# Kernel tuning notes

Hardware: AMD Instinct MI355X
Metric: run time of the kernel (lower is better)

The kernel has to match this reference:

```python
import jax, jax.numpy as jnp
from jax import lax
import numpy as np

FEAT_STRIDE = 16
RATIOS = np.array([0.5, 1.0, 2.0])
SCALES = np.array([8.0, 16.0, 32.0])
PRE_NMS = 6000
POST_NMS = 300
NMS_THRESH = 0.7
MIN_SIZE = 16.0
A = 9  # num anchors per location


def _whctrs(a):
    w = a[2] - a[0] + 1.0
    h = a[3] - a[1] + 1.0
    return w, h, a[0] + 0.5 * (w - 1.0), a[1] + 0.5 * (h - 1.0)


def _mkanchors(ws, hs, cx, cy):
    return np.stack([cx - 0.5 * (ws - 1.0), cy - 0.5 * (hs - 1.0),
                     cx + 0.5 * (ws - 1.0), cy + 0.5 * (hs - 1.0)], axis=1)


def generate_anchors(base_size=16):
    base = np.array([1.0, 1.0, base_size, base_size]) - 1.0
    w, h, cx, cy = _whctrs(base)
    size = w * h
    ws = np.round(np.sqrt(size / RATIOS))
    hs = np.round(ws * RATIOS)
    ratio_anchors = _mkanchors(ws, hs, cx, cy)
    out = []
    for ra in ratio_anchors:
        w, h, cx, cy = _whctrs(ra)
        out.append(_mkanchors(w * SCALES, h * SCALES, cx, cy))
    return np.concatenate(out, axis=0).astype(np.float32)  # [9,4]


def setup_inputs() -> dict:
    key = jax.random.key(0)
    k1, k2 = jax.random.split(key)
    scores = jax.random.normal(k1, (1, 2 * A, 50, 80), dtype=jnp.float32)
    bbox_deltas = jax.random.normal(k2, (1, 4 * A, 50, 80), dtype=jnp.float32) * 0.5
    im_info = jnp.array([[800.0, 1280.0, 1.5]], dtype=jnp.float32)  # (h, w, scale)
    return {"scores": scores, "bbox_deltas": bbox_deltas, "im_info": im_info}


def reference(scores, bbox_deltas, im_info):
    base_anchors = jnp.asarray(generate_anchors())  # [A,4]
    H, W = scores.shape[-2], scores.shape[-1]

    # fg scores, flattened in (h, w, a) order to match anchor ordering
    sc = scores[:, A:, :, :].transpose(0, 2, 3, 1).reshape(-1)  # [K*A]

    # anchors for every feature-map location
    sx = (jnp.arange(W) * FEAT_STRIDE).astype(jnp.float32)
    sy = (jnp.arange(H) * FEAT_STRIDE).astype(jnp.float32)
    gy, gx = jnp.meshgrid(sy, sx, indexing="ij")
    shifts = jnp.stack([gx, gy, gx, gy], axis=-1).reshape(-1, 1, 4)  # [K,1,4]
    anchors = (base_anchors[None, :, :] + shifts).reshape(-1, 4)    # [K*A,4]

    # decode deltas (dw/dh clamped to [-10,10])
    d = bbox_deltas.transpose(0, 2, 3, 1).reshape(-1, 4)
    d = jnp.concatenate([d[:, :2], jnp.clip(d[:, 2:], -10.0, 10.0)], axis=1)
    aw = anchors[:, 2] - anchors[:, 0] + 1.0
    ah = anchors[:, 3] - anchors[:, 1] + 1.0
    acx = anchors[:, 0] + 0.5 * aw
    acy = anchors[:, 1] + 0.5 * ah
    pcx = d[:, 0] * aw + acx
    pcy = d[:, 1] * ah + acy
    pw = jnp.exp(d[:, 2]) * aw
    ph = jnp.exp(d[:, 3]) * ah
    boxes = jnp.stack([pcx - 0.5 * pw, pcy - 0.5 * ph,
                       pcx + 0.5 * pw, pcy + 0.5 * ph], axis=1)

    # clip to image
    im_h, im_w, im_s = im_info[0, 0], im_info[0, 1], im_info[0, 2]
    boxes = jnp.stack([
        jnp.clip(boxes[:, 0], 0.0, im_w - 1.0),
        jnp.clip(boxes[:, 1], 0.0, im_h - 1.0),
        jnp.clip(boxes[:, 2], 0.0, im_w - 1.0),
        jnp.clip(boxes[:, 3], 0.0, im_h - 1.0),
    ], axis=1)

    # min-size filter (masking instead of compaction, for static shapes)
    ws = boxes[:, 2] - boxes[:, 0] + 1.0
    hs = boxes[:, 3] - boxes[:, 1] + 1.0
    min_sz = MIN_SIZE * im_s
    valid = (ws >= min_sz) & (hs >= min_sz)
    sc = jnp.where(valid, sc, -jnp.inf)

    # pre-NMS top-k by score
    top_sc, top_idx = lax.top_k(sc, PRE_NMS)
    props = boxes[top_idx]  # [P,4], sorted by descending score
    alive0 = jnp.isfinite(top_sc)

    # pairwise IoU (the +1 pixel convention matching the rest of the pipeline)
    x1, y1, x2, y2 = props[:, 0], props[:, 1], props[:, 2], props[:, 3]
    areas = (x2 - x1 + 1.0) * (y2 - y1 + 1.0)
    iw = jnp.clip(jnp.minimum(x2[:, None], x2[None, :]) - jnp.maximum(x1[:, None], x1[None, :]) + 1.0, 0.0)
    ih = jnp.clip(jnp.minimum(y2[:, None], y2[None, :]) - jnp.maximum(y1[:, None], y1[None, :]) + 1.0, 0.0)
    inter = iw * ih
    iou = inter / (areas[:, None] + areas[None, :] - inter)  # [P,P] ~144MB

    idx = jnp.arange(PRE_NMS)

    def body(i, keep):
        sup = keep[i] & (iou[i] > NMS_THRESH) & (idx > i)
        return keep & ~sup

    keep = lax.fori_loop(0, PRE_NMS, body, alive0)

    # gather first POST_NMS kept proposals into fixed-size output [POST_NMS,5]
    rank = jnp.cumsum(keep) - 1
    dest = jnp.where(keep & (rank < POST_NMS), rank, POST_NMS)
    out = jnp.zeros((POST_NMS + 1, 5), dtype=scores.dtype)
    out = out.at[dest, 1:].set(props)
    return out[:POST_NMS]
```

## Files before the change

### kernel.cpp

```cpp
#include <hip/hip_runtime.h>
#include <stdint.h>

#define A_NUM 9
#define H_FM 50
#define W_FM 80
#define HW (H_FM * W_FM)
#define N_ANCH (A_NUM * HW)
#define PRE_NMS_N 6000
#define POST_NMS_N 300
#define NMS_TH 0.7f
#define MASK_W 94
#define NPAIR 47
#define MASK_STRIDE 96
#define NBIN 4096
#define BIN_CAP 4096
#define NBD 141
#define MASK_TILES (24 * 94)

typedef unsigned long long ull;

__constant__ float c_aw[9] = {184.f,368.f,736.f,128.f,256.f,512.f, 88.f,176.f,352.f};
__constant__ float c_ah[9] = { 96.f,192.f,384.f,128.f,256.f,512.f,176.f,352.f,704.f};

__device__ int    g_hist[NBIN];
__device__ ull    g_dead[MASK_STRIDE];
__device__ ull    g_rowany[MASK_STRIDE];
__device__ float4 g_boxes[N_ANCH];
__device__ float4 g_props[PRE_NMS_N];
__device__ ull    g_mask[(size_t)PRE_NMS_N * MASK_STRIDE];
__device__ ull    g_colsup[MASK_W * 64];
__device__ ull    g_csup[NPAIR * 64];

__device__ __forceinline__ float iou_gt(float4 bi, float ai, float4 bj, float aj) {
    float iw = fminf(bi.z, bj.z) - fmaxf(bi.x, bj.x) + 1.f;
    float ih = fminf(bi.w, bj.w) - fmaxf(bi.y, bj.y) + 1.f;
    iw = fmaxf(iw, 0.f);
    ih = fmaxf(ih, 0.f);
    float inter = iw * ih;
    return inter / (ai + aj - inter);
}

__global__ __launch_bounds__(256) void k_decode(const float* __restrict__ scores,
                                                const float* __restrict__ deltas,
                                                const float* __restrict__ iminfo,
                                                ull* __restrict__ bins) {
    int t = blockIdx.x * 256 + threadIdx.x;
    if (t >= N_ANCH) return;
    int a    = t / HW;
    int cell = t - a * HW;
    int x    = cell % W_FM;
    int y    = cell / W_FM;

    float sc = scores[(A_NUM + a) * HW + cell];

    int dbase = (a * 4) * HW + cell;
    float d0 = deltas[dbase];
    float d1 = deltas[dbase + HW];
    float d2 = deltas[dbase + 2 * HW];
    float d3 = deltas[dbase + 3 * HW];
    d2 = fminf(fmaxf(d2, -10.f), 10.f);
    d3 = fminf(fmaxf(d3, -10.f), 10.f);

    float aw = c_aw[a], ah = c_ah[a];
    float acx = (float)(x * 16 + 8);
    float acy = (float)(y * 16 + 8);

    float pcx = d0 * aw + acx;
    float pcy = d1 * ah + acy;
    float pw  = expf(d2) * aw;
    float ph  = expf(d3) * ah;

    float x1 = pcx - 0.5f * pw;
    float y1 = pcy - 0.5f * ph;
    float x2 = pcx + 0.5f * pw;
    float y2 = pcy + 0.5f * ph;

    float imh = iminfo[0], imw = iminfo[1], ims = iminfo[2];
    x1 = fminf(fmaxf(x1, 0.f), imw - 1.f);
    y1 = fminf(fmaxf(y1, 0.f), imh - 1.f);
    x2 = fminf(fmaxf(x2, 0.f), imw - 1.f);
    y2 = fminf(fmaxf(y2, 0.f), imh - 1.f);

    float wsz = x2 - x1 + 1.f;
    float hsz = y2 - y1 + 1.f;
    float minsz = 16.f * ims;
    bool valid = (wsz >= minsz) && (hsz >= minsz);

    g_boxes[t] = make_float4(x1, y1, x2, y2);

    unsigned int u   = __float_as_uint(sc);
    unsigned int asc = (u & 0x80000000u) ? ~u : (u | 0x80000000u);
    unsigned int dk  = ~asc;
    if (!valid) dk = 0xFF800000u;

    unsigned int ikey = (unsigned int)(cell * A_NUM + a);
    ull key = ((ull)dk << 32) | ikey;

    int bin  = (int)(dk >> 20);
    int slot = atomicAdd(&g_hist[bin], 1);
    if (slot < BIN_CAP) bins[(size_t)bin * BIN_CAP + slot] = key;
}

__global__ __launch_bounds__(256) void k_binsort(const ull* __restrict__ bins) {
    __shared__ ull sb[4096];
    __shared__ int red[256];
    int b = blockIdx.x;
    int cntf = g_hist[b];
    if (cntf == 0) return;
    int tid = threadIdx.x;

    int part = 0;
    for (int j = tid; j < b; j += 256) part += g_hist[j];
    red[tid] = part;
    __syncthreads();
    for (int off = 128; off > 0; off >>= 1) {
        if (tid < off) red[tid] += red[tid + off];
        __syncthreads();
    }
    int s0 = red[0];
    if (s0 >= PRE_NMS_N) return;

    int cnt = (cntf < BIN_CAP) ? cntf : BIN_CAP;
    const ull* seg = bins + (size_t)b * BIN_CAP;

    int P = 2; while (P < cnt) P <<= 1;
    for (int i = tid; i < P; i += 256) sb[i] = (i < cnt) ? seg[i] : ~0ULL;
    __syncthreads();
    for (int k2 = 2; k2 <= P; k2 <<= 1) {
        for (int j = k2 >> 1; j >= 1; j >>= 1) {
            for (int p = tid; p < (P >> 1); p += 256) {
                int i  = ((p & ~(j - 1)) << 1) | (p & (j - 1));
                int pr = i | j;
                bool up = ((i & k2) == 0);
                ull a = sb[i], c = sb[pr];
                if ((a > c) == up) { sb[i] = c; sb[pr] = a; }
            }
            __syncthreads();
        }
    }
    for (int i = tid; i < cnt; i += 256) {
        int r = s0 + i;
        if (r < PRE_NMS_N) {
            ull key = sb[i];
            unsigned int dk = (unsigned int)(key >> 32);
            if (dk < 0xFF800000u) {
                unsigned int ik = (unsigned int)key;
                int tt = (int)(ik % A_NUM) * HW + (int)(ik / A_NUM);
                g_props[r] = g_boxes[tt];
            } else {
                g_props[r] = make_float4(0.f, 0.f, 0.f, 0.f);
                atomicOr(&g_dead[r >> 6], 1ULL << (r & 63));
            }
        }
    }
}

__global__ __launch_bounds__(256) void k_maskcol() {
    __shared__ float4 sj[256];
    int vb = blockIdx.x;
    int tid = threadIdx.x;

    if (vb < 16) g_hist[vb * 256 + tid] = 0;

    if (vb < MASK_TILES) {
        int bx = vb % 24;
        int by = vb / 24;

        int li = tid & 63;
        int wl = tid >> 6;
        int i  = by * 64 + li;
        int w  = bx * 4 + wl;

        if (bx * 256 + 255 <= by * 64) {
            if (i < PRE_NMS_N && w < MASK_W)
                g_mask[(size_t)i * MASK_STRIDE + w] = 0ULL;
            return;
        }

        int jbase = bx * 256;
        int jj = jbase + tid;
        sj[tid] = (jj < PRE_NMS_N) ? g_props[jj] : make_float4(0.f, 0.f, 0.f, 0.f);
        __syncthreads();

        if (i >= PRE_NMS_N || w >= MASK_W) return;

        float4 bi = g_props[i];
        float ai = (bi.z - bi.x + 1.f) * (bi.w - bi.y + 1.f);
        ull bits = 0;
        int jstart = w * 64;
        int lbase = jstart - jbase;
        int bstart = i + 1 - jstart; if (bstart < 0) bstart = 0;
        int bend = PRE_NMS_N - jstart; if (bend > 64) bend = 64;
        for (int b = bstart; b < bend; ++b) {
            float4 bj = sj[lbase + b];
            float aj = (bj.z - bj.x + 1.f) * (bj.w - bj.y + 1.f);
            if (iou_gt(bi, ai, bj, aj) > NMS_TH) bits |= (1ULL << b);
        }
        g_mask[(size_t)i * MASK_STRIDE + w] = bits;
        int wi = i >> 6;
        bool instep = (w == wi) || (((wi & 1) == 0) && (w == wi + 1));
        if (bits && !instep) atomicOr(&g_rowany[wi], 1ULL << (i & 63));
    } else {
        int w = vb - MASK_TILES;
        int gj = w * 64 + tid;
        if (tid < 64)
            sj[tid] = (gj < PRE_NMS_N) ? g_props[gj] : make_float4(0.f, 0.f, 0.f, 0.f);
        if ((w & 1) && tid >= 64 && tid < 128) {
            int gj2 = (w - 1) * 64 + (tid - 64);
            sj[tid] = (gj2 < PRE_NMS_N) ? g_props[gj2] : make_float4(0.f, 0.f, 0.f, 0.f);
        }
        __syncthreads();
        if (tid < 64) {
            float4 bj = sj[tid];
            float aj = (bj.z - bj.x + 1.f) * (bj.w - bj.y + 1.f);
            ull bits = 0;
            for (int b = 0; b < tid; ++b) {
                float4 bi = sj[b];
                float ai = (bi.z - bi.x + 1.f) * (bi.w - bi.y + 1.f);
                if (iou_gt(bi, ai, bj, aj) > NMS_TH) bits |= (1ULL << b);
            }
            g_colsup[gj] = bits;
            if (w & 1) {
                ull cb = 0;
                for (int b = 0; b < 64; ++b) {
                    float4 bi = sj[64 + b];
                    float ai = (bi.z - bi.x + 1.f) * (bi.w - bi.y + 1.f);
                    if (iou_gt(bi, ai, bj, aj) > NMS_TH) cb |= (1ULL << b);
                }
                g_csup[(w >> 1) * 64 + tid] = cb;
            }
        }
    }
}

#define BATCH 8
__global__ __launch_bounds__(256, 1) void k_scan(float* __restrict__ out) {
    __shared__ ull scol[MASK_W * 64];
    __shared__ ull scsup[NPAIR * 64];
    __shared__ ull srow[MASK_W];
    __shared__ int s_kept[POST_NMS_N];
    __shared__ int s_kc;
    int tid = threadIdx.x;

    for (int i = tid; i < MASK_W * 64; i += 256) scol[i] = g_colsup[i];
    for (int i = tid; i < NPAIR * 64; i += 256)  scsup[i] = g_csup[i];
    for (int i = tid; i < MASK_W; i += 256)      srow[i] = g_rowany[i];
    __syncthreads();

    if (tid < 64) {
        int lane = tid;
        ull rm0 = g_dead[lane];
        ull rm1 = (lane < MASK_W - 64) ? g_dead[64 + lane] : ~0ULL;
        if (lane == 29) rm1 |= 0xFFFF000000000000ULL;
        int kc = 0;
        int ps = -2;
        ull pA = 0, pB = 0, pC = 0;

        for (;;) {
            ull avail0 = __ballot(~rm0 != 0ULL);
            ull avail1 = __ballot(~rm1 != 0ULL);
            int w;
            if (avail0)      w = __ffsll(avail0) - 1;
            else if (avail1) w = 63 + __ffsll(avail1);
            else break;

            int s  = w >> 1;
            int w0 = s << 1;
            int w1 = w0 | 1;

            ull diagA, diagB, csup;
            if (s == ps + 1) { diagA = pA; diagB = pB; csup = pC; }
            else {
                diagA = scol[(w0 << 6) + lane];
                diagB = scol[(w1 << 6) + lane];
                csup  = scsup[(s << 6) + lane];
            }
            if (s + 1 < NPAIR) {
                pA = scol[((w0 + 2) << 6) + lane];
                pB = scol[((w1 + 2) << 6) + lane];
                pC = scsup[((s + 1) << 6) + lane];
            }
            ps = s;

            ull raw0 = srow[w0], raw1 = srow[w1];

            ull rmw0 = (w0 < 64) ? rm0 : rm1;
            int ri0  = (w0 < 64) ? w0 : w0 - 64;
            ull curw0 = ((ull)__builtin_amdgcn_readlane((unsigned)(rmw0 >> 32), ri0) << 32)
                        | __builtin_amdgcn_readlane((unsigned)rmw0, ri0);
            ull rmw1 = (w1 < 64) ? rm0 : rm1;
            int ri1  = (w1 < 64) ? w1 : w1 - 64;
            ull curw1 = ((ull)__builtin_amdgcn_readlane((unsigned)(rmw1 >> 32), ri1) << 32)
                        | __builtin_amdgcn_readlane((unsigned)rmw1, ri1);

            ull U = ~curw0, K0 = 0;
            while (U) {
                ull UK = U | K0;
                bool deadp = (diagA & K0) != 0ULL;
                bool freep = (diagA & UK) == 0ULL;
                ull nd = __ballot(deadp) & U;
                U &= ~nd;
                ull nk = __ballot(freep) & U;
                U &= ~nk;
                K0 |= nk;
                if (!nk && !nd) break;
            }

            ull U1 = ~curw1;
            U1 &= ~__ballot((csup & K0) != 0ULL);
            ull K1 = 0;
            while (U1) {
                ull UK = U1 | K1;
                bool deadp = (diagB & K1) != 0ULL;
                bool freep = (diagB & UK) == 0ULL;
                ull nd = __ballot(deadp) & U1;
                U1 &= ~nd;
                ull nk = __ballot(freep) & U1;
                U1 &= ~nk;
                K1 |= nk;
                if (!nk && !nd) break;
            }

            int cnt0 = __popcll(K0);
            int take0 = min(cnt0, POST_NMS_N - kc);
            if (K0 & (1ULL << lane)) {
                int pos = kc + __popcll(K0 & ((1ULL << lane) - 1ULL));
                if (pos < POST_NMS_N) s_kept[pos] = (w0 << 6) + lane;
            }
            kc += take0;
            if (kc >= POST_NMS_N) break;

            int cnt1 = __popcll(K1);
            int take1 = min(cnt1, POST_NMS_N - kc);
            if (K1 & (1ULL << lane)) {
                int pos = kc + __popcll(K1 & ((1ULL << lane) - 1ULL));
                if (pos < POST_NMS_N) s_kept[pos] = (w1 << 6) + lane;
            }
            kc += take1;
            if (kc >= POST_NMS_N) break;

            if (w0 < 64) { if (lane == w0)      rm0 = ~0ULL; }
            else         { if (lane == w0 - 64) rm1 = ~0ULL; }
            if (w1 < 64) { if (lane == w1)      rm0 = ~0ULL; }
            else         { if (lane == w1 - 64) rm1 = ~0ULL; }

            ull needA = K0 & raw0;
            ull needB = K1 & raw1;
            while (needA | needB) {
                int id[BATCH];
                int n = 0;
#pragma unroll
                for (int t2 = 0; t2 < BATCH; ++t2) {
                    id[t2] = 0;
                    if (needA) {
                        int b = __ffsll(needA) - 1; needA &= needA - 1;
                        id[t2] = (w0 << 6) + b; n = t2 + 1;
                    } else if (needB) {
                        int b = __ffsll(needB) - 1; needB &= needB - 1;
                        id[t2] = (w1 << 6) + b; n = t2 + 1;
                    }
                }
                ull v0[BATCH], v1[BATCH];
#pragma unroll
                for (int t2 = 0; t2 < BATCH; ++t2) {
                    const ull* __restrict__ row =
                        g_mask + (size_t)id[t2] * MASK_STRIDE;
                    v0[t2] = row[lane];
                    v1[t2] = (lane < MASK_W - 64) ? row[64 + lane] : 0ULL;
                }
                ull a0 = 0, a1 = 0;
#pragma unroll
                for (int t2 = 0; t2 < BATCH; ++t2) {
                    ull m = (t2 < n) ? ~0ULL : 0ULL;
                    a0 |= v0[t2] & m;
                    a1 |= v1[t2] & m;
                }
                rm0 |= a0;
                rm1 |= a1;
            }
        }
        if (lane == 0) s_kc = (kc < POST_NMS_N) ? kc : POST_NMS_N;
    }
    __syncthreads();

    for (int i = tid; i < MASK_STRIDE; i += 256) {
        g_dead[i] = 0ULL;
        g_rowany[i] = 0ULL;
    }

    int kcf = s_kc;
    for (int r = tid; r < POST_NMS_N; r += 256) {
        float4 p = make_float4(0.f, 0.f, 0.f, 0.f);
        if (r < kcf) p = g_props[s_kept[r]];
        out[r * 5 + 0] = 0.f;
        out[r * 5 + 1] = p.x;
        out[r * 5 + 2] = p.y;
        out[r * 5 + 3] = p.z;
        out[r * 5 + 4] = p.w;
    }
}

extern "C" void kernel_launch(void* const* d_in, const int* in_sizes, int n_in,
                              void* d_out, int out_size, void* d_ws, size_t ws_size,
                              hipStream_t stream) {
    const float* scores = (const float*)d_in[0];
    const float* deltas = (const float*)d_in[1];
    const float* iminfo = (const float*)d_in[2];
    float* out = (float*)d_out;
    ull* bins = (ull*)d_ws;

    k_decode<<<NBD, 256, 0, stream>>>(scores, deltas, iminfo, bins);
    k_binsort<<<NBIN, 256, 0, stream>>>(bins);
    k_maskcol<<<MASK_TILES + MASK_W, 256, 0, stream>>>();
    k_scan<<<1, 256, 0, stream>>>(out);
}
```

Before: 122.3 us.

## Remap mask tile threads, precompute areas in LDS, aggregate row flags

Rearranges the IoU mask tile kernel so each group of four adjacent threads handles one row across four 64-bit mask words. This makes the global mask stores contiguous. Candidate box areas are computed once into a padded shared array instead of being recomputed inside every inner loop. Lower-triangle tiles now exit without writing zeros, which relies on those mask entries staying zero from static initialisation. Per-row any-suppression bits are gathered with a shared-memory atomic and flushed once per block, instead of one global atomic per thread.

Measured after the change: 119.5 us. -2.3%, faster.

```diff
diff --git a/kernel.cpp b/kernel.cpp
--- a/kernel.cpp
+++ b/kernel.cpp
@@ -31,7 +31,7 @@
 __device__ ull    g_colsup[MASK_W * 64];
 __device__ ull    g_csup[NPAIR * 64];
 
-__device__ __forceinline__ float iou_gt(float4 bi, float ai, float4 bj, float aj) {
+__device__ __forceinline__ float iou_of(float4 bi, float ai, float4 bj, float aj) {
     float iw = fminf(bi.z, bj.z) - fmaxf(bi.x, bj.x) + 1.f;
     float ih = fminf(bi.w, bj.w) - fmaxf(bi.y, bj.y) + 1.f;
     iw = fmaxf(iw, 0.f);
@@ -156,7 +156,9 @@
 }
 
 __global__ __launch_bounds__(256) void k_maskcol() {
-    __shared__ float4 sj[256];
+    __shared__ float4 sj[4 * 65];
+    __shared__ float  sa[4 * 65];
+    __shared__ ull    s_row;
     int vb = blockIdx.x;
     int tid = threadIdx.x;
 
@@ -166,40 +168,43 @@
         int bx = vb % 24;
         int by = vb / 24;
 
-        int li = tid & 63;
-        int wl = tid >> 6;
+        if (bx * 256 + 255 <= by * 64) return;
+
+        if (tid == 0) s_row = 0ULL;
+
+        int li = tid >> 2;
+        int wl = tid & 3;
         int i  = by * 64 + li;
         int w  = bx * 4 + wl;
 
-        if (bx * 256 + 255 <= by * 64) {
-            if (i < PRE_NMS_N && w < MASK_W)
-                g_mask[(size_t)i * MASK_STRIDE + w] = 0ULL;
-            return;
-        }
-
+        int q = tid >> 6, r = tid & 63;
         int jbase = bx * 256;
-        int jj = jbase + tid;
-        sj[tid] = (jj < PRE_NMS_N) ? g_props[jj] : make_float4(0.f, 0.f, 0.f, 0.f);
+        int jj = jbase + q * 64 + r;
+        float4 bjs = (jj < PRE_NMS_N) ? g_props[jj] : make_float4(0.f, 0.f, 0.f, 0.f);
+        sj[q * 65 + r] = bjs;
+        sa[q * 65 + r] = (bjs.z - bjs.x + 1.f) * (bjs.w - bjs.y + 1.f);
         __syncthreads();
 
-        if (i >= PRE_NMS_N || w >= MASK_W) return;
-
-        float4 bi = g_props[i];
-        float ai = (bi.z - bi.x + 1.f) * (bi.w - bi.y + 1.f);
+        bool act = (i < PRE_NMS_N) && (w < MASK_W);
         ull bits = 0;
-        int jstart = w * 64;
-        int lbase = jstart - jbase;
-        int bstart = i + 1 - jstart; if (bstart < 0) bstart = 0;
-        int bend = PRE_NMS_N - jstart; if (bend > 64) bend = 64;
-        for (int b = bstart; b < bend; ++b) {
-            float4 bj = sj[lbase + b];
-            float aj = (bj.z - bj.x + 1.f) * (bj.w - bj.y + 1.f);
-            if (iou_gt(bi, ai, bj, aj) > NMS_TH) bits |= (1ULL << b);
-        }
-        g_mask[(size_t)i * MASK_STRIDE + w] = bits;
+        if (act) {
+            float4 bi = g_props[i];
+            float ai = (bi.z - bi.x + 1.f) * (bi.w - bi.y + 1.f);
+            int jstart = w * 64;
+            int bstart = i + 1 - jstart; if (bstart < 0) bstart = 0;
+            int bend = PRE_NMS_N - jstart; if (bend > 64) bend = 64;
+            const float4* sw = &sj[wl * 65];
+            const float*  swa = &sa[wl * 65];
+            for (int b = bstart; b < bend; ++b) {
+                if (iou_of(bi, ai, sw[b], swa[b]) > NMS_TH) bits |= (1ULL << b);
+            }
+            g_mask[(size_t)i * MASK_STRIDE + w] = bits;
+        }
         int wi = i >> 6;
         bool instep = (w == wi) || (((wi & 1) == 0) && (w == wi + 1));
-        if (bits && !instep) atomicOr(&g_rowany[wi], 1ULL << (i & 63));
+        if (act && bits && !instep) atomicOr(&s_row, 1ULL << (i & 63));
+        __syncthreads();
+        if (tid == 0 && s_row) atomicOr(&g_rowany[by], s_row);
     } else {
         int w = vb - MASK_TILES;
         int gj = w * 64 + tid;
@@ -217,7 +222,7 @@
             for (int b = 0; b < tid; ++b) {
                 float4 bi = sj[b];
                 float ai = (bi.z - bi.x + 1.f) * (bi.w - bi.y + 1.f);
-                if (iou_gt(bi, ai, bj, aj) > NMS_TH) bits |= (1ULL << b);
+                if (iou_of(bi, ai, bj, aj) > NMS_TH) bits |= (1ULL << b);
             }
             g_colsup[gj] = bits;
             if (w & 1) {
@@ -225,7 +230,7 @@
                 for (int b = 0; b < 64; ++b) {
                     float4 bi = sj[64 + b];
                     float ai = (bi.z - bi.x + 1.f) * (bi.w - bi.y + 1.f);
-                    if (iou_gt(bi, ai, bj, aj) > NMS_TH) cb |= (1ULL << b);
+                    if (iou_of(bi, ai, bj, aj) > NMS_TH) cb |= (1ULL << b);
                 }
                 g_csup[(w >> 1) * 64 + tid] = cb;
             }
```
